# Kernel optimization log

Hardware: AMD Instinct MI355X
Metric: run time of the kernel (lower is better)

The kernel has to match this reference:

```python
import jax, jax.numpy as jnp
import numpy as np

IN_DIM = 1024
OUT_DIM = 128
N = 8192


def setup_inputs() -> dict:
    key = jax.random.key(0)
    ks = jax.random.split(key, 7)
    s = 1.0 / np.sqrt(IN_DIM)
    return {
        "z": jax.random.normal(ks[0], (N, IN_DIM), dtype=jnp.float32),
        "Wq": jax.random.normal(ks[1], (IN_DIM, OUT_DIM), dtype=jnp.float32) * s,
        "bq": jax.random.normal(ks[2], (OUT_DIM,), dtype=jnp.float32) * 0.01,
        "Wk": jax.random.normal(ks[3], (IN_DIM, OUT_DIM), dtype=jnp.float32) * s,
        "bk": jax.random.normal(ks[4], (OUT_DIM,), dtype=jnp.float32) * 0.01,
        "Wv": jax.random.normal(ks[5], (IN_DIM, OUT_DIM), dtype=jnp.float32) * s,
        "bv": jax.random.normal(ks[6], (OUT_DIM,), dtype=jnp.float32) * 0.01,
    }


def reference(z, Wq, bq, Wk, bk, Wv, bv):
    # QKV projections: [N, in_dim] @ [in_dim, out_dim] + bias -> [N, out_dim]
    q = z @ Wq + bq
    k = z @ Wk + bk
    v = z @ Wv + bv
    dh = q.shape[-1]
    # Scores [N, N], scaled by sqrt(dh); softmax over last axis (torch 2-D default)
    scores = (q @ k.T) * (1.0 / jnp.sqrt(jnp.asarray(dh, q.dtype)))
    A = jax.nn.softmax(scores, axis=-1)
    return A @ v
```

## Files before the change

### kernel.cpp

```cpp
#include <hip/hip_runtime.h>


#define N_TOK   8192
#define D_IN    1024
#define D_HEAD  128
#define QSCALE  (0.08838834764831845f * 1.4426950408889634f)
#define SPLIT   8
#define QB      128
#define KVB     64
#define NIT     ((N_TOK / SPLIT) / KVB)

typedef _Float16 half8 __attribute__((ext_vector_type(8)));
typedef _Float16 half4 __attribute__((ext_vector_type(4)));
typedef float f32x4 __attribute__((ext_vector_type(4)));

__global__ void prep_wt(const float* __restrict__ Wq, const float* __restrict__ Wk,
                        const float* __restrict__ Wv, _Float16* __restrict__ Wt) {
    int i = blockIdx.x * 256 + threadIdx.x;
    int mat = i >> 17;
    int rem = i & 131071;
    int n = rem >> 10;
    int c = rem & 1023;
    const float* W = (mat == 0) ? Wq : (mat == 1) ? Wk : Wv;
    float v = W[c * 128 + n];
    if (mat == 0) v *= QSCALE;
    Wt[i] = (_Float16)v;
}

__launch_bounds__(256)
__global__ void qkv_gemm(const float* __restrict__ z, const _Float16* __restrict__ Wt,
                         const float* __restrict__ bq, const float* __restrict__ bk,
                         const float* __restrict__ bv,
                         _Float16* __restrict__ Qs, _Float16* __restrict__ Kh,
                         _Float16* __restrict__ Vt) {
    __shared__ __align__(16) _Float16 A_lds[64 * 72];
    __shared__ __align__(16) _Float16 B_lds[128 * 72];
    const int mat = blockIdx.y;
    const int m0 = blockIdx.x * 64;
    const int t = threadIdx.x;
    const int lane = t & 63, w = t >> 6;
    const int l15 = lane & 15, g = lane >> 4;
    const _Float16* Wm = Wt + (size_t)mat * 131072;

    f32x4 acc[8] = {};

    const int arow = t >> 2, aseg = t & 3;
    const int bn = t >> 1, bh = t & 1;

    for (int c0 = 0; c0 < D_IN; c0 += 64) {
        const float4* zp = reinterpret_cast<const float4*>(
            z + (size_t)(m0 + arow) * D_IN + c0 + aseg * 16);
        float4 f0 = zp[0], f1 = zp[1], f2 = zp[2], f3 = zp[3];
        const half8* wp = reinterpret_cast<const half8*>(Wm + (size_t)bn * D_IN + c0 + bh * 32);
        half8 w0 = wp[0], w1 = wp[1], w2 = wp[2], w3 = wp[3];

        __syncthreads();

        half8 h0, h1;
        h0[0]=(_Float16)f0.x; h0[1]=(_Float16)f0.y; h0[2]=(_Float16)f0.z; h0[3]=(_Float16)f0.w;
        h0[4]=(_Float16)f1.x; h0[5]=(_Float16)f1.y; h0[6]=(_Float16)f1.z; h0[7]=(_Float16)f1.w;
        h1[0]=(_Float16)f2.x; h1[1]=(_Float16)f2.y; h1[2]=(_Float16)f2.z; h1[3]=(_Float16)f2.w;
        h1[4]=(_Float16)f3.x; h1[5]=(_Float16)f3.y; h1[6]=(_Float16)f3.z; h1[7]=(_Float16)f3.w;
        *reinterpret_cast<half8*>(&A_lds[arow * 72 + aseg * 16])     = h0;
        *reinterpret_cast<half8*>(&A_lds[arow * 72 + aseg * 16 + 8]) = h1;
        half8* bd = reinterpret_cast<half8*>(&B_lds[bn * 72 + bh * 32]);
        bd[0] = w0; bd[1] = w1; bd[2] = w2; bd[3] = w3;

        __syncthreads();

        half8 a0 = *reinterpret_cast<half8*>(&A_lds[(w * 16 + l15) * 72 + g * 8]);
        half8 a1 = *reinterpret_cast<half8*>(&A_lds[(w * 16 + l15) * 72 + 32 + g * 8]);
#pragma unroll
        for (int nt = 0; nt < 8; nt++) {
            half8 b0 = *reinterpret_cast<half8*>(&B_lds[(nt * 16 + l15) * 72 + g * 8]);
            half8 b1 = *reinterpret_cast<half8*>(&B_lds[(nt * 16 + l15) * 72 + 32 + g * 8]);
            acc[nt] = __builtin_amdgcn_mfma_f32_16x16x32_f16(a0, b0, acc[nt], 0, 0, 0);
            acc[nt] = __builtin_amdgcn_mfma_f32_16x16x32_f16(a1, b1, acc[nt], 0, 0, 0);
        }
    }

    const float* bias = (mat == 0) ? bq : (mat == 1) ? bk : bv;
    if (mat < 2) {
        _Float16* dst = (mat == 0) ? Qs : Kh;
#pragma unroll
        for (int nt = 0; nt < 8; nt++) {
            float b = bias[nt * 16 + l15];
            if (mat == 0) b *= QSCALE;
#pragma unroll
            for (int r = 0; r < 4; r++) {
                int m = m0 + w * 16 + g * 4 + r;
                dst[(size_t)m * D_HEAD + nt * 16 + l15] = (_Float16)(acc[nt][r] + b);
            }
        }
    } else {
#pragma unroll
        for (int nt = 0; nt < 8; nt++) {
            float b = bias[nt * 16 + l15];
            half4 pk;
#pragma unroll
            for (int r = 0; r < 4; r++) pk[r] = (_Float16)(acc[nt][r] + b);
            int m = m0 + w * 16 + g * 4;
            *reinterpret_cast<half4*>(&Vt[(size_t)(nt * 16 + l15) * N_TOK + m]) = pk;
        }
    }
}

__launch_bounds__(256, 2)
__global__ void attn(const _Float16* __restrict__ Qs, const _Float16* __restrict__ Kh,
                     const _Float16* __restrict__ Vt,
                     _Float16* __restrict__ Opart, float* __restrict__ lpart) {
    __shared__ __align__(16) char lds[49152];
    char* Kb = lds;
    char* Vb = lds + 16384;
    char* Pb = lds + 32768;

    const int t = threadIdx.x;
    const int lane = t & 63, w = t >> 6;
    const int l15 = lane & 15, g = lane >> 4;
    const int q0 = blockIdx.x * QB;
    const int sp = blockIdx.y;
    const int kvA = sp * (N_TOK / SPLIT);

    half8 qa[2][4];
#pragma unroll
    for (int r16 = 0; r16 < 2; r16++)
#pragma unroll
        for (int ct = 0; ct < 4; ct++)
            qa[r16][ct] = *reinterpret_cast<const half8*>(
                Qs + (size_t)(q0 + w * 32 + r16 * 16 + l15) * D_HEAD + ct * 32 + g * 8);

    const int krow = t >> 2, kseg = t & 3;
    const int vd = t >> 1, vh = t & 1;
    int kw[4], vw[4];
#pragma unroll
    for (int i = 0; i < 4; i++) {
        kw[i] = krow * 256 + (((kseg * 4 + i) ^ (krow & 7)) << 4);
        vw[i] = vd * 128 + (((vh * 4 + i) ^ (vd & 7)) << 4);
    }
    int kru[4], vru[2];
#pragma unroll
    for (int ct = 0; ct < 4; ct++) kru[ct] = ((ct * 4 + g) ^ (l15 & 7)) << 4;
#pragma unroll
    for (int s2 = 0; s2 < 2; s2++) vru[s2] = ((s2 * 4 + g) ^ (l15 & 7)) << 4;
    char* Pw = Pb + w * 4096;
    const int phi = l15 >> 3, plo = (l15 & 7) * 2;
    int px[4];
#pragma unroll
    for (int r = 0; r < 4; r++) px[r] = (g * 4 + r) & 7;

    f32x4 o[2][8] = {};
    float lsum[2][4] = {};

    const _Float16* kg = Kh + (size_t)(kvA + krow) * D_HEAD + kseg * 32;
    const _Float16* vg = Vt + (size_t)vd * N_TOK + kvA + vh * 32;
    half8 kr[4], vr[4];
#pragma unroll
    for (int i = 0; i < 4; i++) {
        kr[i] = reinterpret_cast<const half8*>(kg)[i];
        vr[i] = reinterpret_cast<const half8*>(vg)[i];
    }

    for (int it = 0; it < NIT; ++it) {
        __syncthreads();
#pragma unroll
        for (int i = 0; i < 4; i++) {
            *reinterpret_cast<half8*>(Kb + kw[i]) = kr[i];
            *reinterpret_cast<half8*>(Vb + vw[i]) = vr[i];
        }
        __syncthreads();

        if (it + 1 < NIT) {
            kg += (size_t)KVB * D_HEAD;
            vg += KVB;
#pragma unroll
            for (int i = 0; i < 4; i++) {
                kr[i] = reinterpret_cast<const half8*>(kg)[i];
                vr[i] = reinterpret_cast<const half8*>(vg)[i];
            }
        }

        f32x4 sf[2][4] = {};
        __builtin_amdgcn_s_setprio(1);
#pragma unroll
        for (int kt = 0; kt < 4; kt++) {
#pragma unroll
            for (int ct = 0; ct < 4; ct++) {
                half8 kf = *reinterpret_cast<half8*>(Kb + kt * 4096 + l15 * 256 + kru[ct]);
#pragma unroll
                for (int r16 = 0; r16 < 2; r16++)
                    sf[r16][kt] = __builtin_amdgcn_mfma_f32_16x16x32_f16(
                        qa[r16][ct], kf, sf[r16][kt], 0, 0, 0);
            }
        }
        __builtin_amdgcn_s_setprio(0);

#pragma unroll
        for (int r16 = 0; r16 < 2; r16++)
#pragma unroll
            for (int kt = 0; kt < 4; kt++)
#pragma unroll
                for (int r = 0; r < 4; r++) {
                    float p = __builtin_amdgcn_exp2f(sf[r16][kt][r]);
                    lsum[r16][r] += p;
                    *reinterpret_cast<_Float16*>(
                        Pw + r16 * 2048 + (g * 4 + r) * 128 +
                        (((kt * 2 + phi) ^ px[r]) << 4) + plo) = (_Float16)p;
                }

        __builtin_amdgcn_s_setprio(1);
#pragma unroll
        for (int s2 = 0; s2 < 2; s2++) {
            half8 pa[2];
#pragma unroll
            for (int r16 = 0; r16 < 2; r16++)
                pa[r16] = *reinterpret_cast<half8*>(Pw + r16 * 2048 + l15 * 128 + vru[s2]);
#pragma unroll
            for (int dt = 0; dt < 8; dt++) {
                half8 vf = *reinterpret_cast<half8*>(Vb + dt * 2048 + l15 * 128 + vru[s2]);
#pragma unroll
                for (int r16 = 0; r16 < 2; r16++)
                    o[r16][dt] = __builtin_amdgcn_mfma_f32_16x16x32_f16(
                        pa[r16], vf, o[r16][dt], 0, 0, 0);
            }
        }
        __builtin_amdgcn_s_setprio(0);
    }

#pragma unroll
    for (int r16 = 0; r16 < 2; r16++)
#pragma unroll
        for (int r = 0; r < 4; r++) {
            float v = lsum[r16][r];
            v += __shfl_xor(v, 1, 64);
            v += __shfl_xor(v, 2, 64);
            v += __shfl_xor(v, 4, 64);
            v += __shfl_xor(v, 8, 64);
            lsum[r16][r] = v;
        }

    _Float16* Op = Opart + (size_t)sp * N_TOK * D_HEAD;
#pragma unroll
    for (int r16 = 0; r16 < 2; r16++)
#pragma unroll
        for (int dt = 0; dt < 8; dt++)
#pragma unroll
            for (int r = 0; r < 4; r++)
                Op[(size_t)(q0 + w * 32 + r16 * 16 + g * 4 + r) * D_HEAD + dt * 16 + l15] =
                    (_Float16)o[r16][dt][r];
    if (l15 == 0) {
#pragma unroll
        for (int r16 = 0; r16 < 2; r16++)
#pragma unroll
            for (int r = 0; r < 4; r++)
                lpart[sp * N_TOK + q0 + w * 32 + r16 * 16 + g * 4 + r] = lsum[r16][r];
    }
}

__global__ void combine(const _Float16* __restrict__ Opart, const float* __restrict__ lpart,
                        float* __restrict__ out) {
    int i = blockIdx.x * 256 + threadIdx.x;
    int base = i * 8;
    int m = base >> 7;
    float acc[8] = {};
    float den = 0.f;
#pragma unroll
    for (int s = 0; s < SPLIT; s++) {
        half8 h = *reinterpret_cast<const half8*>(
            Opart + (size_t)s * N_TOK * D_HEAD + base);
#pragma unroll
        for (int j = 0; j < 8; j++) acc[j] += (float)h[j];
        den += lpart[s * N_TOK + m];
    }
    float inv = 1.f / den;
    float4 o0, o1;
    o0.x = acc[0]*inv; o0.y = acc[1]*inv; o0.z = acc[2]*inv; o0.w = acc[3]*inv;
    o1.x = acc[4]*inv; o1.y = acc[5]*inv; o1.z = acc[6]*inv; o1.w = acc[7]*inv;
    reinterpret_cast<float4*>(out + base)[0] = o0;
    reinterpret_cast<float4*>(out + base)[1] = o1;
}

extern "C" void kernel_launch(void* const* d_in, const int* in_sizes, int n_in,
                              void* d_out, int out_size, void* d_ws, size_t ws_size,
                              hipStream_t stream) {
    const float* z  = (const float*)d_in[0];
    const float* Wq = (const float*)d_in[1];
    const float* bq = (const float*)d_in[2];
    const float* Wk = (const float*)d_in[3];
    const float* bk = (const float*)d_in[4];
    const float* Wv = (const float*)d_in[5];
    const float* bv = (const float*)d_in[6];
    float* out = (float*)d_out;

    char* ws = (char*)d_ws;
    _Float16* Wt = (_Float16*)(ws);
    _Float16* Qs = (_Float16*)(ws + 786432);
    _Float16* Kh = (_Float16*)(ws + 786432 + 2097152);
    _Float16* Vt = (_Float16*)(ws + 786432 + 2 * 2097152);
    _Float16* Opart = (_Float16*)(ws + 786432 + 3 * 2097152);
    float* lpart = (float*)(ws + 786432 + 3 * 2097152 +
                            (size_t)SPLIT * N_TOK * D_HEAD * 2);

    prep_wt<<<1536, 256, 0, stream>>>(Wq, Wk, Wv, Wt);
    qkv_gemm<<<dim3(128, 3), 256, 0, stream>>>(z, Wt, bq, bk, bv, Qs, Kh, Vt);
    attn<<<dim3(N_TOK / QB, SPLIT), 256, 0, stream>>>(Qs, Kh, Vt, Opart, lpart);
    combine<<<512, 256, 0, stream>>>(Opart, lpart, out);
}
```

Before: 149.6 us.

## Retile QKV GEMM to 128x128 with register prefetch and swizzled LDS, transpose weights via LDS

The QKV projection GEMM now uses 128-row tiles with a 2x2 warp layout (4x4 MFMA tiles per warp), doubling A-tile reuse. It prefetches the next K-slice from global memory into registers while the current slice is computed, and uses XOR-swizzled LDS instead of padding. The weight transpose kernel goes through a shared-memory tile so reads and writes are coalesced. The trade-off is that the GEMM launches only 192 blocks with higher register pressure, which may underfill the GPU.

```diff
diff --git a/kernel.cpp b/kernel.cpp
--- a/kernel.cpp
+++ b/kernel.cpp
@@ -16,15 +16,37 @@
 
 __global__ void prep_wt(const float* __restrict__ Wq, const float* __restrict__ Wk,
                         const float* __restrict__ Wv, _Float16* __restrict__ Wt) {
-    int i = blockIdx.x * 256 + threadIdx.x;
-    int mat = i >> 17;
-    int rem = i & 131071;
-    int n = rem >> 10;
-    int c = rem & 1023;
+    __shared__ float T[32][129];
+    const int mat = blockIdx.y;
+    const int k0 = blockIdx.x * 32;
+    const int t = threadIdx.x;
     const float* W = (mat == 0) ? Wq : (mat == 1) ? Wk : Wv;
-    float v = W[c * 128 + n];
-    if (mat == 0) v *= QSCALE;
-    Wt[i] = (_Float16)v;
+
+    const int krow = t >> 3, nc0 = (t & 7) * 16;
+#pragma unroll
+    for (int i = 0; i < 4; i++) {
+        float4 f = reinterpret_cast<const float4*>(
+            W + (size_t)(k0 + krow) * D_HEAD + nc0)[i];
+        T[krow][nc0 + i * 4 + 0] = f.x;
+        T[krow][nc0 + i * 4 + 1] = f.y;
+        T[krow][nc0 + i * 4 + 2] = f.z;
+        T[krow][nc0 + i * 4 + 3] = f.w;
+    }
+    __syncthreads();
+
+    const int n = t >> 1, kh = (t & 1) * 16;
+    half8 h0, h1;
+#pragma unroll
+    for (int j = 0; j < 8; j++) {
+        float v0 = T[kh + j][n];
+        float v1 = T[kh + 8 + j][n];
+        if (mat == 0) { v0 *= QSCALE; v1 *= QSCALE; }
+        h0[j] = (_Float16)v0;
+        h1[j] = (_Float16)v1;
+    }
+    _Float16* dst = Wt + (size_t)mat * 131072 + (size_t)n * D_IN + k0 + kh;
+    reinterpret_cast<half8*>(dst)[0] = h0;
+    reinterpret_cast<half8*>(dst)[1] = h1;
 }
 
 __launch_bounds__(256)
@@ -33,74 +55,117 @@
                          const float* __restrict__ bv,
                          _Float16* __restrict__ Qs, _Float16* __restrict__ Kh,
                          _Float16* __restrict__ Vt) {
-    __shared__ __align__(16) _Float16 A_lds[64 * 72];
-    __shared__ __align__(16) _Float16 B_lds[128 * 72];
+    __shared__ __align__(16) char lds[32768];
+    char* Ab = lds;
+    char* Bb = lds + 16384;
+
     const int mat = blockIdx.y;
-    const int m0 = blockIdx.x * 64;
+    const int m0 = blockIdx.x * 128;
     const int t = threadIdx.x;
     const int lane = t & 63, w = t >> 6;
     const int l15 = lane & 15, g = lane >> 4;
+    const int wm = w >> 1, wn = w & 1;
     const _Float16* Wm = Wt + (size_t)mat * 131072;
 
-    f32x4 acc[8] = {};
-
-    const int arow = t >> 2, aseg = t & 3;
-    const int bn = t >> 1, bh = t & 1;
-
-    for (int c0 = 0; c0 < D_IN; c0 += 64) {
-        const float4* zp = reinterpret_cast<const float4*>(
-            z + (size_t)(m0 + arow) * D_IN + c0 + aseg * 16);
-        float4 f0 = zp[0], f1 = zp[1], f2 = zp[2], f3 = zp[3];
-        const half8* wp = reinterpret_cast<const half8*>(Wm + (size_t)bn * D_IN + c0 + bh * 32);
-        half8 w0 = wp[0], w1 = wp[1], w2 = wp[2], w3 = wp[3];
-
+    const int srow = t >> 1, sh = t & 1;
+    int aw[4], bw[4];
+#pragma unroll
+    for (int i = 0; i < 4; i++) {
+        int u = ((sh * 4 + i) ^ (srow & 7)) << 4;
+        aw[i] = srow * 128 + u;
+        bw[i] = srow * 128 + u;
+    }
+    int ru[2];
+#pragma unroll
+    for (int ct = 0; ct < 2; ct++) ru[ct] = ((ct * 4 + g) ^ (l15 & 7)) << 4;
+
+    f32x4 acc[4][4] = {};
+
+    const float4* zg = reinterpret_cast<const float4*>(
+        z + (size_t)(m0 + srow) * D_IN + sh * 32);
+    const half8* wg = reinterpret_cast<const half8*>(
+        Wm + (size_t)srow * D_IN + sh * 32);
+
+    float4 af[8];
+    half8 bf[4];
+#pragma unroll
+    for (int i = 0; i < 8; i++) af[i] = zg[i];
+#pragma unroll
+    for (int i = 0; i < 4; i++) bf[i] = wg[i];
+
+    for (int it = 0; it < 16; ++it) {
         __syncthreads();
-
-        half8 h0, h1;
-        h0[0]=(_Float16)f0.x; h0[1]=(_Float16)f0.y; h0[2]=(_Float16)f0.z; h0[3]=(_Float16)f0.w;
-        h0[4]=(_Float16)f1.x; h0[5]=(_Float16)f1.y; h0[6]=(_Float16)f1.z; h0[7]=(_Float16)f1.w;
-        h1[0]=(_Float16)f2.x; h1[1]=(_Float16)f2.y; h1[2]=(_Float16)f2.z; h1[3]=(_Float16)f2.w;
-        h1[4]=(_Float16)f3.x; h1[5]=(_Float16)f3.y; h1[6]=(_Float16)f3.z; h1[7]=(_Float16)f3.w;
-        *reinterpret_cast<half8*>(&A_lds[arow * 72 + aseg * 16])     = h0;
-        *reinterpret_cast<half8*>(&A_lds[arow * 72 + aseg * 16 + 8]) = h1;
-        half8* bd = reinterpret_cast<half8*>(&B_lds[bn * 72 + bh * 32]);
-        bd[0] = w0; bd[1] = w1; bd[2] = w2; bd[3] = w3;
-
+#pragma unroll
+        for (int j = 0; j < 4; j++) {
+            half8 h;
+            float4 lo = af[2 * j], hi = af[2 * j + 1];
+            h[0]=(_Float16)lo.x; h[1]=(_Float16)lo.y; h[2]=(_Float16)lo.z; h[3]=(_Float16)lo.w;
+            h[4]=(_Float16)hi.x; h[5]=(_Float16)hi.y; h[6]=(_Float16)hi.z; h[7]=(_Float16)hi.w;
+            *reinterpret_cast<half8*>(Ab + aw[j]) = h;
+            *reinterpret_cast<half8*>(Bb + bw[j]) = bf[j];
+        }
         __syncthreads();
 
-        half8 a0 = *reinterpret_cast<half8*>(&A_lds[(w * 16 + l15) * 72 + g * 8]);
-        half8 a1 = *reinterpret_cast<half8*>(&A_lds[(w * 16 + l15) * 72 + 32 + g * 8]);
-#pragma unroll
-        for (int nt = 0; nt < 8; nt++) {
-            half8 b0 = *reinterpret_cast<half8*>(&B_lds[(nt * 16 + l15) * 72 + g * 8]);
-            half8 b1 = *reinterpret_cast<half8*>(&B_lds[(nt * 16 + l15) * 72 + 32 + g * 8]);
-            acc[nt] = __builtin_amdgcn_mfma_f32_16x16x32_f16(a0, b0, acc[nt], 0, 0, 0);
-            acc[nt] = __builtin_amdgcn_mfma_f32_16x16x32_f16(a1, b1, acc[nt], 0, 0, 0);
-        }
+        if (it < 15) {
+            zg += 16;
+            wg += 8;
+#pragma unroll
+            for (int i = 0; i < 8; i++) af[i] = zg[i];
+#pragma unroll
+            for (int i = 0; i < 4; i++) bf[i] = wg[i];
+        }
+
+        __builtin_amdgcn_s_setprio(1);
+#pragma unroll
+        for (int ct = 0; ct < 2; ct++) {
+            half8 afr[4], bfr[4];
+#pragma unroll
+            for (int m16 = 0; m16 < 4; m16++)
+                afr[m16] = *reinterpret_cast<half8*>(
+                    Ab + (wm * 64 + m16 * 16 + l15) * 128 + ru[ct]);
+#pragma unroll
+            for (int n16 = 0; n16 < 4; n16++)
+                bfr[n16] = *reinterpret_cast<half8*>(
+                    Bb + (wn * 64 + n16 * 16 + l15) * 128 + ru[ct]);
+#pragma unroll
+            for (int m16 = 0; m16 < 4; m16++)
+#pragma unroll
+                for (int n16 = 0; n16 < 4; n16++)
+                    acc[m16][n16] = __builtin_amdgcn_mfma_f32_16x16x32_f16(
+                        afr[m16], bfr[n16], acc[m16][n16], 0, 0, 0);
+        }
+        __builtin_amdgcn_s_setprio(0);
     }
 
     const float* bias = (mat == 0) ? bq : (mat == 1) ? bk : bv;
     if (mat < 2) {
         _Float16* dst = (mat == 0) ? Qs : Kh;
 #pragma unroll
-        for (int nt = 0; nt < 8; nt++) {
-            float b = bias[nt * 16 + l15];
+        for (int n16 = 0; n16 < 4; n16++) {
+            int n = wn * 64 + n16 * 16 + l15;
+            float b = bias[n];
             if (mat == 0) b *= QSCALE;
 #pragma unroll
-            for (int r = 0; r < 4; r++) {
-                int m = m0 + w * 16 + g * 4 + r;
-                dst[(size_t)m * D_HEAD + nt * 16 + l15] = (_Float16)(acc[nt][r] + b);
+            for (int m16 = 0; m16 < 4; m16++)
+#pragma unroll
+                for (int r = 0; r < 4; r++) {
+                    int m = m0 + wm * 64 + m16 * 16 + g * 4 + r;
+                    dst[(size_t)m * D_HEAD + n] = (_Float16)(acc[m16][n16][r] + b);
+                }
+        }
+    } else {
+#pragma unroll
+        for (int n16 = 0; n16 < 4; n16++) {
+            int n = wn * 64 + n16 * 16 + l15;
+            float b = bias[n];
+#pragma unroll
+            for (int m16 = 0; m16 < 4; m16++) {
+                half4 pk;
+#pragma unroll
+                for (int r = 0; r < 4; r++) pk[r] = (_Float16)(acc[m16][n16][r] + b);
+                int m = m0 + wm * 64 + m16 * 16 + g * 4;
+                *reinterpret_cast<half4*>(&Vt[(size_t)n * N_TOK + m]) = pk;
             }
-        }
-    } else {
-#pragma unroll
-        for (int nt = 0; nt < 8; nt++) {
-            float b = bias[nt * 16 + l15];
-            half4 pk;
-#pragma unroll
-            for (int r = 0; r < 4; r++) pk[r] = (_Float16)(acc[nt][r] + b);
-            int m = m0 + w * 16 + g * 4;
-            *reinterpret_cast<half4*>(&Vt[(size_t)(nt * 16 + l15) * N_TOK + m]) = pk;
         }
     }
 }
@@ -300,8 +365,8 @@
     float* lpart = (float*)(ws + 786432 + 3 * 2097152 +
                             (size_t)SPLIT * N_TOK * D_HEAD * 2);
 
-    prep_wt<<<1536, 256, 0, stream>>>(Wq, Wk, Wv, Wt);
-    qkv_gemm<<<dim3(128, 3), 256, 0, stream>>>(z, Wt, bq, bk, bv, Qs, Kh, Vt);
+    prep_wt<<<dim3(32, 3), 256, 0, stream>>>(Wq, Wk, Wv, Wt);
+    qkv_gemm<<<dim3(64, 3), 256, 0, stream>>>(z, Wt, bq, bk, bv, Qs, Kh, Vt);
     attn<<<dim3(N_TOK / QB, SPLIT), 256, 0, stream>>>(Qs, Kh, Vt, Opart, lpart);
     combine<<<512, 256, 0, stream>>>(Opart, lpart, out);
 }
```

After: 159.7 us. +6.7%, slower.

## Enlarge attention Q tile, transpose MFMA operands, raise KV split, tile weight prep

Applied to the files above, without the earlier changes.

The attention kernel now handles 256 query rows per block (64 per wave), so each K/V tile loaded into LDS is reused across twice as many queries. The MFMA operands are swapped so each lane keeps a full row of scores, which gives packed half stores of P, a simpler lsum reduction and vectorized output writes. The KV split goes from 8 to 16 when workspace allows. Register prefetch of the next K/V tile is removed, and prep_wt is rewritten as an LDS-tiled transpose with vector loads. The larger tile raises register and LDS pressure and may reduce occupancy, and the wider split makes the combine step read more partial results.

```diff
diff --git a/kernel.cpp b/kernel.cpp
--- a/kernel.cpp
+++ b/kernel.cpp
@@ -5,26 +5,50 @@
 #define D_IN    1024
 #define D_HEAD  128
 #define QSCALE  (0.08838834764831845f * 1.4426950408889634f)
-#define SPLIT   8
-#define QB      128
 #define KVB     64
-#define NIT     ((N_TOK / SPLIT) / KVB)
 
 typedef _Float16 half8 __attribute__((ext_vector_type(8)));
 typedef _Float16 half4 __attribute__((ext_vector_type(4)));
 typedef float f32x4 __attribute__((ext_vector_type(4)));
 
+static __device__ __forceinline__ int pkrtz(float a, float b) {
+    auto h = __builtin_amdgcn_cvt_pkrtz(a, b);
+    return __builtin_bit_cast(int, h);
+}
+
 __global__ void prep_wt(const float* __restrict__ Wq, const float* __restrict__ Wk,
                         const float* __restrict__ Wv, _Float16* __restrict__ Wt) {
-    int i = blockIdx.x * 256 + threadIdx.x;
-    int mat = i >> 17;
-    int rem = i & 131071;
-    int n = rem >> 10;
-    int c = rem & 1023;
+    __shared__ float T[32][129];
+    const int mat = blockIdx.y;
+    const int k0 = blockIdx.x * 32;
+    const int t = threadIdx.x;
     const float* W = (mat == 0) ? Wq : (mat == 1) ? Wk : Wv;
-    float v = W[c * 128 + n];
-    if (mat == 0) v *= QSCALE;
-    Wt[i] = (_Float16)v;
+
+    const int krow = t >> 3, nc0 = (t & 7) * 16;
+#pragma unroll
+    for (int i = 0; i < 4; i++) {
+        float4 f = reinterpret_cast<const float4*>(
+            W + (size_t)(k0 + krow) * D_HEAD + nc0)[i];
+        T[krow][nc0 + i * 4 + 0] = f.x;
+        T[krow][nc0 + i * 4 + 1] = f.y;
+        T[krow][nc0 + i * 4 + 2] = f.z;
+        T[krow][nc0 + i * 4 + 3] = f.w;
+    }
+    __syncthreads();
+
+    const int n = t >> 1, kh = (t & 1) * 16;
+    half8 h0, h1;
+#pragma unroll
+    for (int j = 0; j < 8; j++) {
+        float v0 = T[kh + j][n];
+        float v1 = T[kh + 8 + j][n];
+        if (mat == 0) { v0 *= QSCALE; v1 *= QSCALE; }
+        h0[j] = (_Float16)v0;
+        h1[j] = (_Float16)v1;
+    }
+    _Float16* dst = Wt + (size_t)mat * 131072 + (size_t)n * D_IN + k0 + kh;
+    reinterpret_cast<half8*>(dst)[0] = h0;
+    reinterpret_cast<half8*>(dst)[1] = h1;
 }
 
 __launch_bounds__(256)
@@ -105,29 +129,32 @@
     }
 }
 
+template <int SPLIT>
 __launch_bounds__(256, 2)
 __global__ void attn(const _Float16* __restrict__ Qs, const _Float16* __restrict__ Kh,
                      const _Float16* __restrict__ Vt,
                      _Float16* __restrict__ Opart, float* __restrict__ lpart) {
-    __shared__ __align__(16) char lds[49152];
-    char* Kb = lds;
-    char* Vb = lds + 16384;
-    char* Pb = lds + 32768;
+    constexpr int NIT = (N_TOK / SPLIT) / KVB;
+    __shared__ __align__(16) char lds[69632];
 
     const int t = threadIdx.x;
     const int lane = t & 63, w = t >> 6;
     const int l15 = lane & 15, g = lane >> 4;
-    const int q0 = blockIdx.x * QB;
+    const int q0 = blockIdx.x * 256;
     const int sp = blockIdx.y;
     const int kvA = sp * (N_TOK / SPLIT);
 
-    half8 qa[2][4];
-#pragma unroll
-    for (int r16 = 0; r16 < 2; r16++)
+    char* Kb = lds;
+    char* Vb = lds + 16384;
+    char* Pw = lds + 32768 + w * 9216;
+
+    half8 qa[4][4];
+#pragma unroll
+    for (int qg = 0; qg < 4; qg++)
 #pragma unroll
         for (int ct = 0; ct < 4; ct++)
-            qa[r16][ct] = *reinterpret_cast<const half8*>(
-                Qs + (size_t)(q0 + w * 32 + r16 * 16 + l15) * D_HEAD + ct * 32 + g * 8);
+            qa[qg][ct] = *reinterpret_cast<const half8*>(
+                Qs + (size_t)(q0 + w * 64 + qg * 16 + l15) * D_HEAD + ct * 32 + g * 8);
 
     const int krow = t >> 2, kseg = t & 3;
     const int vd = t >> 1, vh = t & 1;
@@ -141,26 +168,24 @@
 #pragma unroll
     for (int ct = 0; ct < 4; ct++) kru[ct] = ((ct * 4 + g) ^ (l15 & 7)) << 4;
 #pragma unroll
-    for (int s2 = 0; s2 < 2; s2++) vru[s2] = ((s2 * 4 + g) ^ (l15 & 7)) << 4;
-    char* Pw = Pb + w * 4096;
-    const int phi = l15 >> 3, plo = (l15 & 7) * 2;
-    int px[4];
-#pragma unroll
-    for (int r = 0; r < 4; r++) px[r] = (g * 4 + r) & 7;
-
-    f32x4 o[2][8] = {};
-    float lsum[2][4] = {};
+    for (int ks = 0; ks < 2; ks++) vru[ks] = ((ks * 4 + g) ^ (l15 & 7)) << 4;
+
+    f32x4 o[4][8] = {};
+    float lsum[4] = {};
 
     const _Float16* kg = Kh + (size_t)(kvA + krow) * D_HEAD + kseg * 32;
     const _Float16* vg = Vt + (size_t)vd * N_TOK + kvA + vh * 32;
-    half8 kr[4], vr[4];
-#pragma unroll
-    for (int i = 0; i < 4; i++) {
-        kr[i] = reinterpret_cast<const half8*>(kg)[i];
-        vr[i] = reinterpret_cast<const half8*>(vg)[i];
-    }
 
     for (int it = 0; it < NIT; ++it) {
+        half8 kr[4], vr[4];
+#pragma unroll
+        for (int i = 0; i < 4; i++) {
+            kr[i] = reinterpret_cast<const half8*>(kg)[i];
+            vr[i] = reinterpret_cast<const half8*>(vg)[i];
+        }
+        kg += (size_t)KVB * D_HEAD;
+        vg += KVB;
+
         __syncthreads();
 #pragma unroll
         for (int i = 0; i < 4; i++) {
@@ -169,93 +194,80 @@
         }
         __syncthreads();
 
-        if (it + 1 < NIT) {
-            kg += (size_t)KVB * D_HEAD;
-            vg += KVB;
-#pragma unroll
-            for (int i = 0; i < 4; i++) {
-                kr[i] = reinterpret_cast<const half8*>(kg)[i];
-                vr[i] = reinterpret_cast<const half8*>(vg)[i];
+        __builtin_amdgcn_s_setprio(1);
+#pragma unroll
+        for (int kt = 0; kt < 4; kt++) {
+            f32x4 sf[4] = {};
+#pragma unroll
+            for (int ct = 0; ct < 4; ct++) {
+                half8 kf = *reinterpret_cast<half8*>(
+                    Kb + (kt * 16 + l15) * 256 + kru[ct]);
+#pragma unroll
+                for (int qg = 0; qg < 4; qg++)
+                    sf[qg] = __builtin_amdgcn_mfma_f32_16x16x32_f16(
+                        kf, qa[qg][ct], sf[qg], 0, 0, 0);
             }
-        }
-
-        f32x4 sf[2][4] = {};
-        __builtin_amdgcn_s_setprio(1);
-#pragma unroll
-        for (int kt = 0; kt < 4; kt++) {
-#pragma unroll
-            for (int ct = 0; ct < 4; ct++) {
-                half8 kf = *reinterpret_cast<half8*>(Kb + kt * 4096 + l15 * 256 + kru[ct]);
-#pragma unroll
-                for (int r16 = 0; r16 < 2; r16++)
-                    sf[r16][kt] = __builtin_amdgcn_mfma_f32_16x16x32_f16(
-                        qa[r16][ct], kf, sf[r16][kt], 0, 0, 0);
+#pragma unroll
+            for (int qg = 0; qg < 4; qg++) {
+                float e0 = __builtin_amdgcn_exp2f(sf[qg][0]);
+                float e1 = __builtin_amdgcn_exp2f(sf[qg][1]);
+                float e2 = __builtin_amdgcn_exp2f(sf[qg][2]);
+                float e3 = __builtin_amdgcn_exp2f(sf[qg][3]);
+                lsum[qg] += (e0 + e1) + (e2 + e3);
+                char* pp = Pw + (qg * 16 + l15) * 144 + kt * 32 + g * 8;
+                *reinterpret_cast<int*>(pp)     = pkrtz(e0, e1);
+                *reinterpret_cast<int*>(pp + 4) = pkrtz(e2, e3);
             }
         }
+
+#pragma unroll
+        for (int ks = 0; ks < 2; ks++) {
+            half8 pa[4];
+#pragma unroll
+            for (int qg = 0; qg < 4; qg++)
+                pa[qg] = *reinterpret_cast<half8*>(
+                    Pw + (qg * 16 + l15) * 144 + ks * 64 + g * 16);
+#pragma unroll
+            for (int dt = 0; dt < 8; dt++) {
+                half8 vf = *reinterpret_cast<half8*>(
+                    Vb + (dt * 16 + l15) * 128 + vru[ks]);
+#pragma unroll
+                for (int qg = 0; qg < 4; qg++)
+                    o[qg][dt] = __builtin_amdgcn_mfma_f32_16x16x32_f16(
+                        vf, pa[qg], o[qg][dt], 0, 0, 0);
+            }
+        }
         __builtin_amdgcn_s_setprio(0);
-
-#pragma unroll
-        for (int r16 = 0; r16 < 2; r16++)
-#pragma unroll
-            for (int kt = 0; kt < 4; kt++)
-#pragma unroll
-                for (int r = 0; r < 4; r++) {
-                    float p = __builtin_amdgcn_exp2f(sf[r16][kt][r]);
-                    lsum[r16][r] += p;
-                    *reinterpret_cast<_Float16*>(
-                        Pw + r16 * 2048 + (g * 4 + r) * 128 +
-                        (((kt * 2 + phi) ^ px[r]) << 4) + plo) = (_Float16)p;
-                }
-
-        __builtin_amdgcn_s_setprio(1);
-#pragma unroll
-        for (int s2 = 0; s2 < 2; s2++) {
-            half8 pa[2];
-#pragma unroll
-            for (int r16 = 0; r16 < 2; r16++)
-                pa[r16] = *reinterpret_cast<half8*>(Pw + r16 * 2048 + l15 * 128 + vru[s2]);
-#pragma unroll
-            for (int dt = 0; dt < 8; dt++) {
-                half8 vf = *reinterpret_cast<half8*>(Vb + dt * 2048 + l15 * 128 + vru[s2]);
-#pragma unroll
-                for (int r16 = 0; r16 < 2; r16++)
-                    o[r16][dt] = __builtin_amdgcn_mfma_f32_16x16x32_f16(
-                        pa[r16], vf, o[r16][dt], 0, 0, 0);
-            }
-        }
-        __builtin_amdgcn_s_setprio(0);
-    }
-
-#pragma unroll
-    for (int r16 = 0; r16 < 2; r16++)
-#pragma unroll
-        for (int r = 0; r < 4; r++) {
-            float v = lsum[r16][r];
-            v += __shfl_xor(v, 1, 64);
-            v += __shfl_xor(v, 2, 64);
-            v += __shfl_xor(v, 4, 64);
-            v += __shfl_xor(v, 8, 64);
-            lsum[r16][r] = v;
-        }
+    }
+
+#pragma unroll
+    for (int qg = 0; qg < 4; qg++) {
+        float v = lsum[qg];
+        v += __shfl_xor(v, 16, 64);
+        v += __shfl_xor(v, 32, 64);
+        lsum[qg] = v;
+    }
 
     _Float16* Op = Opart + (size_t)sp * N_TOK * D_HEAD;
 #pragma unroll
-    for (int r16 = 0; r16 < 2; r16++)
-#pragma unroll
-        for (int dt = 0; dt < 8; dt++)
-#pragma unroll
-            for (int r = 0; r < 4; r++)
-                Op[(size_t)(q0 + w * 32 + r16 * 16 + g * 4 + r) * D_HEAD + dt * 16 + l15] =
-                    (_Float16)o[r16][dt][r];
-    if (l15 == 0) {
-#pragma unroll
-        for (int r16 = 0; r16 < 2; r16++)
-#pragma unroll
-            for (int r = 0; r < 4; r++)
-                lpart[sp * N_TOK + q0 + w * 32 + r16 * 16 + g * 4 + r] = lsum[r16][r];
-    }
-}
-
+    for (int qg = 0; qg < 4; qg++) {
+        const size_t qrow = (size_t)(q0 + w * 64 + qg * 16 + l15) * D_HEAD;
+#pragma unroll
+        for (int dt = 0; dt < 8; dt++) {
+            int2 pv;
+            pv.x = pkrtz(o[qg][dt][0], o[qg][dt][1]);
+            pv.y = pkrtz(o[qg][dt][2], o[qg][dt][3]);
+            *reinterpret_cast<int2*>(Op + qrow + dt * 16 + g * 4) = pv;
+        }
+    }
+    if (lane < 16) {
+#pragma unroll
+        for (int qg = 0; qg < 4; qg++)
+            lpart[sp * N_TOK + q0 + w * 64 + qg * 16 + l15] = lsum[qg];
+    }
+}
+
+template <int SPLIT>
 __global__ void combine(const _Float16* __restrict__ Opart, const float* __restrict__ lpart,
                         float* __restrict__ out) {
     int i = blockIdx.x * 256 + threadIdx.x;
@@ -297,11 +309,18 @@
     _Float16* Kh = (_Float16*)(ws + 786432 + 2097152);
     _Float16* Vt = (_Float16*)(ws + 786432 + 2 * 2097152);
     _Float16* Opart = (_Float16*)(ws + 786432 + 3 * 2097152);
-    float* lpart = (float*)(ws + 786432 + 3 * 2097152 +
-                            (size_t)SPLIT * N_TOK * D_HEAD * 2);
-
-    prep_wt<<<1536, 256, 0, stream>>>(Wq, Wk, Wv, Wt);
+
+    prep_wt<<<dim3(32, 3), 256, 0, stream>>>(Wq, Wk, Wv, Wt);
     qkv_gemm<<<dim3(128, 3), 256, 0, stream>>>(z, Wt, bq, bk, bv, Qs, Kh, Vt);
-    attn<<<dim3(N_TOK / QB, SPLIT), 256, 0, stream>>>(Qs, Kh, Vt, Opart, lpart);
-    combine<<<512, 256, 0, stream>>>(Opart, lpart, out);
-}
+
+    const size_t need16 = 786432 + 3 * 2097152ull + 16 * 2097152ull + 16 * N_TOK * 4ull;
+    if (ws_size >= need16) {
+        float* lpart = (float*)(ws + 786432 + 3 * 2097152 + 16 * 2097152ull);
+        attn<16><<<dim3(32, 16), 256, 0, stream>>>(Qs, Kh, Vt, Opart, lpart);
+        combine<16><<<512, 256, 0, stream>>>(Opart, lpart, out);
+    } else {
+        float* lpart = (float*)(ws + 786432 + 3 * 2097152 + 8 * 2097152ull);
+        attn<8><<<dim3(32, 8), 256, 0, stream>>>(Qs, Kh, Vt, Opart, lpart);
+        combine<8><<<512, 256, 0, stream>>>(Opart, lpart, out);
+    }
+}
```

After: 203.2 us. +35.8%, slower.
